# Kernel tuning notes

Measured on AMD Instinct MI355X. Metric: run time of the kernel, lower is better.

The kernel has to match this reference:

```python
import jax, jax.numpy as jnp
import numpy as np

B, T, C, L = 1024, 256, 128, 64
NEG = -1e30  # finite stand-in for -inf (safe gradients)
EPS = 1e-7   # keras.backend.epsilon()


def setup_inputs() -> dict:
    key = jax.random.key(0)
    k1, k2 = jax.random.split(key)
    # y_pred is a softmax output (probabilities), as keras ctc_batch_cost expects
    logits = jax.random.normal(k1, (B, T, C), dtype=jnp.float32)
    y_pred = jax.nn.softmax(logits, axis=-1)
    # labels in [0, C-2]; class C-1 is the CTC blank (keras convention)
    y_true = jax.random.randint(k2, (B, L), 0, C - 1, dtype=jnp.int64)
    return {"y_true": y_true, "y_pred": y_pred}


def ctc_loss(y_true, y_pred):
    """Negative log-likelihood CTC loss per sample, shape [B, 1].
    Matches keras.backend.ctc_batch_cost with full input/label lengths,
    blank index = num_classes - 1, log(y_pred + eps)."""
    Bb, Tt, Cc = y_pred.shape
    Ll = y_true.shape[1]
    blank = Cc - 1
    S = 2 * Ll + 1  # extended label: blank, l1, blank, l2, ..., blank

    logp = jnp.log(y_pred + EPS)  # [B, T, C]

    ext = jnp.full((Bb, S), blank, dtype=y_true.dtype).at[:, 1::2].set(y_true)  # [B, S]
    # per-(t, s) log-prob of the extended symbol: lp[b, t, s] = logp[b, t, ext[b, s]]
    lp = jnp.take_along_axis(logp, ext[:, None, :], axis=2)  # [B, T, S]

    # skip transition s-2 -> s allowed iff ext[s] != blank and ext[s] != ext[s-2]
    ext_m2 = jnp.concatenate(
        [jnp.full((Bb, 2), blank, dtype=ext.dtype), ext[:, :-2]], axis=1)
    can_skip = (ext != blank) & (ext != ext_m2)  # [B, S]

    def shift1(a):
        return jnp.concatenate(
            [jnp.full((Bb, 1), NEG, dtype=a.dtype), a[:, :-1]], axis=1)

    # alpha init at t=0: only s=0 (blank) and s=1 (first label) reachable
    alpha0 = (jnp.full((Bb, S), NEG, dtype=lp.dtype)
              .at[:, 0].set(lp[:, 0, 0])
              .at[:, 1].set(lp[:, 0, 1]))

    def step(alpha, lp_t):
        a1 = shift1(alpha)
        a2 = jnp.where(can_skip, shift1(shift1(alpha)), NEG)
        new = jax.nn.logsumexp(jnp.stack([alpha, a1, a2], axis=0), axis=0) + lp_t
        return new, None

    lp_tbs = jnp.swapaxes(lp, 0, 1)  # [T, B, S]
    alpha, _ = jax.lax.scan(step, alpha0, lp_tbs[1:])

    log_lik = jnp.logaddexp(alpha[:, S - 1], alpha[:, S - 2])  # end on last blank or last label
    return -log_lik[:, None]  # [B, 1], matching ctc_batch_cost output shape


def reference(y_true, y_pred):
    return ctc_loss(y_true, y_pred)
```

## Files before the change

### kernel.cpp

```cpp
#include <hip/hip_runtime.h>
#include <math.h>


#define Bn 1024
#define Tn 256
#define Cn 128
#define Ln 64
#define BLANK 127
#define U 8
#define NC (Tn / U)
#define RING 8
#define DEPTH 7
#define EPS128 (1e-7f * 128.0f)
#define LN2 0.69314718055994530942f

#define WAIT_VM(n) __builtin_amdgcn_s_waitcnt((((n) & 0xF) | (((n) >> 4) << 14)) | 0x0F70)
#define SCHED_FENCE() __builtin_amdgcn_sched_barrier(0)

template <int CTRL>
__device__ __forceinline__ float dpp_movf(float x) {
    return __int_as_float(__builtin_amdgcn_update_dpp(
        0, __float_as_int(x), CTRL, 0xF, 0xF, true));
}
__device__ __forceinline__ int dpp_shr1_i(int x) {
    return __builtin_amdgcn_update_dpp(0, x, 0x138, 0xF, 0xF, true);
}
__device__ __forceinline__ void dma16(const float* g, float* l) {
    __builtin_amdgcn_global_load_lds(
        (const __attribute__((address_space(1))) void*)g,
        (__attribute__((address_space(3))) void*)l, 16, 0, 0);
}

__global__ __launch_bounds__(128)
void ctc_ring_kernel(const int* __restrict__ y_true,
                     const float* __restrict__ y_pred,
                     float* __restrict__ out) {
    __shared__ __align__(16) float ring[2][RING][U * Cn];
    const int w = threadIdx.x >> 6;
    const int i = threadIdx.x & 63;
    const int b = blockIdx.x * 2 + w;

    float (*myring)[U * Cn] = ring[w];

    const int li = y_true[b * Ln + i];
    const int ll = dpp_shr1_i(li);
    const float skf = (li != ll) ? 1.0f : 0.0f;

    const float* gb = y_pred + (size_t)b * (Tn * Cn);

    auto issue_chunk = [&](int c) {
        const float* g = gb + c * (U * Cn);
        float* l = myring[c & (RING - 1)];
#pragma unroll
        for (int k = 0; k < 4; ++k)
            dma16(g + k * 256 + i * 4, l + k * 256);
    };

    float qlA[U], qbA[U], qlB[U], qbB[U];
    auto qread = [&](int c, float* ql, float* qb) {
        const float* s = myring[c & (RING - 1)];
#pragma unroll
        for (int j = 0; j < U; ++j) {
            ql[j] = fmaf(s[j * Cn + li],    128.0f, EPS128);
            qb[j] = fmaf(s[j * Cn + BLANK], 128.0f, EPS128);
        }
    };

    float E = 0.f, O = 0.f, X = 0.f;
    int Esum = 0;

    auto steps = [&](const float* ql, const float* qb, bool first) {
#pragma unroll
        for (int j = 0; j < U; ++j) {
            if (first && j == 0) {
                E = (i == 0) ? qb[0] : 0.f;
                O = (i == 0) ? ql[0] : 0.f;
                X = 0.f;
                continue;
            }
            const float Ol = dpp_movf<0x138>(O);
            const float t1 = O + E;
            const float nO = fmaf(skf, Ol, t1) * ql[j];
            const float nE = (E + Ol) * qb[j];
            const float nX = (X + O) * qb[j];
            E = nE; O = nO; X = nX;
        }
    };
    auto renorm = [&]() {
        float m = fmaxf(E, O);
        if (i == 63) m = fmaxf(m, X);
        m = fmaxf(m, dpp_movf<0x111>(m));
        m = fmaxf(m, dpp_movf<0x112>(m));
        m = fmaxf(m, dpp_movf<0x114>(m));
        m = fmaxf(m, dpp_movf<0x118>(m));
        m = fmaxf(m, dpp_movf<0x142>(m));
        m = fmaxf(m, dpp_movf<0x143>(m));
        const unsigned ub =
            (unsigned)__builtin_amdgcn_readlane(__float_as_int(m), 63);
        const int eb = (int)(ub >> 23);
        const float sc = __int_as_float((unsigned)(254 - eb) << 23);
        Esum += eb - 127;
        E *= sc; O *= sc; X *= sc;
    };

#pragma unroll
    for (int c = 0; c < DEPTH; ++c) issue_chunk(c);
    WAIT_VM(24);
    SCHED_FENCE();
    qread(0, qlA, qbA);

    for (int cc = 0; cc < 24; cc += 2) {
        WAIT_VM(20); SCHED_FENCE();
        qread(cc + 1, qlB, qbB);
        issue_chunk(cc + 7);
        steps(qlA, qbA, cc == 0);
        renorm();
        WAIT_VM(20); SCHED_FENCE();
        qread(cc + 2, qlA, qbA);
        issue_chunk(cc + 8);
        steps(qlB, qbB, false);
        renorm();
    }
    WAIT_VM(20); SCHED_FENCE();
    qread(25, qlB, qbB);
    issue_chunk(31);
    steps(qlA, qbA, false);
    renorm();
    WAIT_VM(0); SCHED_FENCE();
    qread(26, qlA, qbA);
    steps(qlB, qbB, false);
    renorm();
    qread(27, qlB, qbB); steps(qlA, qbA, false); renorm();
    qread(28, qlA, qbA); steps(qlB, qbB, false); renorm();
    qread(29, qlB, qbB); steps(qlA, qbA, false); renorm();
    qread(30, qlA, qbA); steps(qlB, qbB, false); renorm();
    qread(31, qlB, qbB); steps(qlA, qbA, false); renorm();
    steps(qlB, qbB, false);

    if (i == 63) {
        const float s = O + X;
#if __has_builtin(__builtin_amdgcn_logf)
        const float l2 = __builtin_amdgcn_logf(s);
#else
        const float l2 = log2f(s);
#endif
        out[b] = -(l2 + (float)(Esum - 7 * Tn)) * LN2;
    }
}

extern "C" void kernel_launch(void* const* d_in, const int* in_sizes, int n_in,
                              void* d_out, int out_size, void* d_ws, size_t ws_size,
                              hipStream_t stream) {
    const int*   y_true = (const int*)d_in[0];
    const float* y_pred = (const float*)d_in[1];
    float*       out    = (float*)d_out;
    hipLaunchKernelGGL(ctc_ring_kernel, dim3(Bn / 2), dim3(128), 0, stream,
                       y_true, y_pred, out);
}
```

Measured before the change: 192.7 us.

## Split each sample across two ping-pong waves exchanging alpha state via LDS

Each block now handles one sample with two waves that take alternating time chunks. Each wave prefetches only its own chunks into a smaller ring, and the recursion state (E, O, X, exponent sum) is handed between waves through shared memory with a barrier after every chunk. The aim is to hide one wave's LDS gather and DMA wait behind the other wave's recurrence. In exchange, every chunk now pays for a barrier and an LDS state round-trip on the serial critical path, and the grid doubles.

```diff
diff --git a/kernel.cpp b/kernel.cpp
--- a/kernel.cpp
+++ b/kernel.cpp
@@ -8,13 +8,13 @@
 #define Ln 64
 #define BLANK 127
 #define U 8
-#define NC (Tn / U)
-#define RING 8
-#define DEPTH 7
+#define KH 16
+#define RING 4
 #define EPS128 (1e-7f * 128.0f)
 #define LN2 0.69314718055994530942f
 
 #define WAIT_VM(n) __builtin_amdgcn_s_waitcnt((((n) & 0xF) | (((n) >> 4) << 14)) | 0x0F70)
+#define WAIT_LGKM() __builtin_amdgcn_s_waitcnt(0xC07F)
 #define SCHED_FENCE() __builtin_amdgcn_sched_barrier(0)
 
 template <int CTRL>
@@ -30,17 +30,24 @@
         (const __attribute__((address_space(1))) void*)g,
         (__attribute__((address_space(3))) void*)l, 16, 0, 0);
 }
+__device__ __forceinline__ void wave_sync() {
+    SCHED_FENCE();
+    WAIT_LGKM();
+    __builtin_amdgcn_s_barrier();
+    SCHED_FENCE();
+}
 
 __global__ __launch_bounds__(128)
-void ctc_ring_kernel(const int* __restrict__ y_true,
+void ctc_pair_kernel(const int* __restrict__ y_true,
                      const float* __restrict__ y_pred,
                      float* __restrict__ out) {
     __shared__ __align__(16) float ring[2][RING][U * Cn];
+    __shared__ float stE[64], stO[64], stX[64];
+    __shared__ int stS;
+
     const int w = threadIdx.x >> 6;
     const int i = threadIdx.x & 63;
-    const int b = blockIdx.x * 2 + w;
-
-    float (*myring)[U * Cn] = ring[w];
+    const int b = blockIdx.x;
 
     const int li = y_true[b * Ln + i];
     const int ll = dpp_shr1_i(li);
@@ -48,17 +55,17 @@
 
     const float* gb = y_pred + (size_t)b * (Tn * Cn);
 
-    auto issue_chunk = [&](int c) {
-        const float* g = gb + c * (U * Cn);
-        float* l = myring[c & (RING - 1)];
+    auto issue = [&](int k) {
+        const float* g = gb + (2 * k + w) * (U * Cn);
+        float* l = ring[w][k & (RING - 1)];
 #pragma unroll
-        for (int k = 0; k < 4; ++k)
-            dma16(g + k * 256 + i * 4, l + k * 256);
+        for (int kk = 0; kk < 4; ++kk)
+            dma16(g + kk * 256 + i * 4, l + kk * 256);
     };
 
-    float qlA[U], qbA[U], qlB[U], qbB[U];
-    auto qread = [&](int c, float* ql, float* qb) {
-        const float* s = myring[c & (RING - 1)];
+    float ql[U], qb[U];
+    auto gather = [&](int k) {
+        const float* s = ring[w][k & (RING - 1)];
 #pragma unroll
         for (int j = 0; j < U; ++j) {
             ql[j] = fmaf(s[j * Cn + li],    128.0f, EPS128);
@@ -69,7 +76,7 @@
     float E = 0.f, O = 0.f, X = 0.f;
     int Esum = 0;
 
-    auto steps = [&](const float* ql, const float* qb, bool first) {
+    auto steps = [&](bool first) {
 #pragma unroll
         for (int j = 0; j < U; ++j) {
             if (first && j == 0) {
@@ -102,49 +109,71 @@
         Esum += eb - 127;
         E *= sc; O *= sc; X *= sc;
     };
+    auto st_write = [&]() {
+        stE[i] = E; stO[i] = O; stX[i] = X;
+        if (i == 63) stS = Esum;
+    };
+    auto st_read = [&]() {
+        E = stE[i]; O = stO[i]; X = stX[i]; Esum = stS;
+    };
 
 #pragma unroll
-    for (int c = 0; c < DEPTH; ++c) issue_chunk(c);
-    WAIT_VM(24);
-    SCHED_FENCE();
-    qread(0, qlA, qbA);
+    for (int k = 0; k < RING; ++k) issue(k);
+    if (w == 0) { WAIT_VM(12); SCHED_FENCE(); gather(0); }
 
-    for (int cc = 0; cc < 24; cc += 2) {
-        WAIT_VM(20); SCHED_FENCE();
-        qread(cc + 1, qlB, qbB);
-        issue_chunk(cc + 7);
-        steps(qlA, qbA, cc == 0);
-        renorm();
-        WAIT_VM(20); SCHED_FENCE();
-        qread(cc + 2, qlA, qbA);
-        issue_chunk(cc + 8);
-        steps(qlB, qbB, false);
-        renorm();
+    for (int k = 0; k < 12; ++k) {
+        if (w == 0) {
+            issue(k + 4);
+            if (k > 0) st_read();
+            steps(k == 0); renorm(); st_write();
+        } else {
+            WAIT_VM(12); SCHED_FENCE();
+            gather(k);
+        }
+        wave_sync();
+        if (w == 1) {
+            issue(k + 4);
+            st_read(); steps(false); renorm(); st_write();
+        } else {
+            WAIT_VM(12); SCHED_FENCE();
+            gather(k + 1);
+        }
+        wave_sync();
     }
-    WAIT_VM(20); SCHED_FENCE();
-    qread(25, qlB, qbB);
-    issue_chunk(31);
-    steps(qlA, qbA, false);
-    renorm();
-    WAIT_VM(0); SCHED_FENCE();
-    qread(26, qlA, qbA);
-    steps(qlB, qbB, false);
-    renorm();
-    qread(27, qlB, qbB); steps(qlA, qbA, false); renorm();
-    qread(28, qlA, qbA); steps(qlB, qbB, false); renorm();
-    qread(29, qlB, qbB); steps(qlA, qbA, false); renorm();
-    qread(30, qlA, qbA); steps(qlB, qbB, false); renorm();
-    qread(31, qlB, qbB); steps(qlA, qbA, false); renorm();
-    steps(qlB, qbB, false);
 
-    if (i == 63) {
-        const float s = O + X;
+    if (w == 0) { st_read(); steps(false); renorm(); st_write(); }
+    else        { WAIT_VM(12); SCHED_FENCE(); gather(12); }
+    wave_sync();
+    if (w == 1) { st_read(); steps(false); renorm(); st_write(); }
+    else        { WAIT_VM(8);  SCHED_FENCE(); gather(13); }
+    wave_sync();
+    if (w == 0) { st_read(); steps(false); renorm(); st_write(); }
+    else        { WAIT_VM(8);  SCHED_FENCE(); gather(13); }
+    wave_sync();
+    if (w == 1) { st_read(); steps(false); renorm(); st_write(); }
+    else        { WAIT_VM(4);  SCHED_FENCE(); gather(14); }
+    wave_sync();
+    if (w == 0) { st_read(); steps(false); renorm(); st_write(); }
+    else        { WAIT_VM(4);  SCHED_FENCE(); gather(14); }
+    wave_sync();
+    if (w == 1) { st_read(); steps(false); renorm(); st_write(); }
+    else        { WAIT_VM(0);  SCHED_FENCE(); gather(15); }
+    wave_sync();
+    if (w == 0) { st_read(); steps(false); renorm(); st_write(); }
+    else        { WAIT_VM(0);  SCHED_FENCE(); gather(15); }
+    wave_sync();
+    if (w == 1) {
+        st_read();
+        steps(false);
+        if (i == 63) {
+            const float s = O + X;
 #if __has_builtin(__builtin_amdgcn_logf)
-        const float l2 = __builtin_amdgcn_logf(s);
+            const float l2 = __builtin_amdgcn_logf(s);
 #else
-        const float l2 = log2f(s);
+            const float l2 = log2f(s);
 #endif
-        out[b] = -(l2 + (float)(Esum - 7 * Tn)) * LN2;
+            out[b] = -(l2 + (float)(Esum - 7 * Tn)) * LN2;
+        }
     }
 }
 
@@ -154,6 +183,6 @@
     const int*   y_true = (const int*)d_in[0];
     const float* y_pred = (const float*)d_in[1];
     float*       out    = (float*)d_out;
-    hipLaunchKernelGGL(ctc_ring_kernel, dim3(Bn / 2), dim3(128), 0, stream,
+    hipLaunchKernelGGL(ctc_pair_kernel, dim3(Bn), dim3(128), 0, stream,
                        y_true, y_pred, out);
 }
```

Result: no change. 194.0 us (+0.7%).
